# Kernel tuning notes

Measured on AMD Instinct MI355X. Metric: run time of the kernel, lower is better.

## Reference

```python
import jax, jax.numpy as jnp
import numpy as np

HS = WS = 1024      # downsampled mask dims (8192 / scale_factor 8)
K = 24              # kernel_num
KD = 35             # kernel_dim1 == kernel_dim2
OFF = HS // 2 - KD // 2  # offset_s = 495
MASK_STEEP = 4.0
MASK_SHIFT = 0.5
RESIST_STEEP = 50.0
RESIST_TH = 0.225
MAX_DOSE = 1.02
MIN_DOSE = 0.98
POOL = 3            # avepool_kernel


def setup_inputs() -> dict:
    key = jax.random.key(0)
    ks = jax.random.split(key, 7)
    return {
        "mask_s": jax.random.uniform(ks[0], (1, 1, HS, WS), dtype=jnp.float32),
        "kf_re": jax.random.normal(ks[1], (K, KD, KD), dtype=jnp.float32),
        "kf_im": jax.random.normal(ks[2], (K, KD, KD), dtype=jnp.float32),
        "kd_re": jax.random.normal(ks[3], (K, KD, KD), dtype=jnp.float32),
        "kd_im": jax.random.normal(ks[4], (K, KD, KD), dtype=jnp.float32),
        "kf_scale": jax.random.uniform(ks[5], (K, 1, 1), dtype=jnp.float32),
        "kd_scale": jax.random.uniform(ks[6], (K, 1, 1), dtype=jnp.float32),
    }


def _avgpool3(x):
    # AvgPool2d(kernel=3, stride=1, pad=1), count_include_pad=True -> always /9
    s = jax.lax.reduce_window(x, 0.0, jax.lax.add, (1, 1, POOL, POOL),
                              (1, 1, 1, 1),
                              [(0, 0), (0, 0), (POOL // 2, POOL // 2), (POOL // 2, POOL // 2)])
    return s / float(POOL * POOL)


def _dose_branch(crop, kernel, scale, dose):
    # crop: [1,1,KD,KD] complex ; kernel: [K,KD,KD] complex ; scale: [K,1,1]
    buf = jnp.zeros((1, K, HS, WS), dtype=jnp.complex64)
    buf = buf.at[:, :, OFF:OFF + KD, OFF:OFF + KD].set(crop * dose * kernel)
    img = jnp.fft.ifft2(buf)                      # [1,K,HS,WS] complex
    inten = (img.real * img.real + img.imag * img.imag) * scale
    inten = jnp.sum(inten, axis=1, keepdims=True)  # [1,1,HS,WS]
    return jax.nn.sigmoid(RESIST_STEEP * (inten - RESIST_TH))


def reference(mask_s, kf_re, kf_im, kd_re, kd_im, kf_scale, kd_scale):
    kf = jax.lax.complex(kf_re, kf_im)
    kd = jax.lax.complex(kd_re, kd_im)
    mask = jax.nn.sigmoid(MASK_STEEP * (_avgpool3(mask_s) - MASK_SHIFT))
    mf = jnp.fft.fftshift(jnp.fft.fft2(mask), axes=(-2, -1))  # [1,1,HS,WS]
    crop = mf[:, :, OFF:OFF + KD, OFF:OFF + KD]               # [1,1,KD,KD]
    x_nom = _dose_branch(crop, kf, kf_scale, 1.0)
    x_max = _dose_branch(crop, kf, kf_scale, MAX_DOSE)
    x_min = _dose_branch(crop, kd, kd_scale, MIN_DOSE)
    return x_nom, x_max, x_min
```

## Files before the change

kernel.cpp:

```cpp
#include <hip/hip_runtime.h>
#include <math.h>

#define HS 1024
#define WS 1024
#define KK 24
#define KD 35
#define NF 35
#define NDP 69
#define NGRP 16
#define CROW 42
#define PROW 37

#define G_OFF    0u
#define CROP_OFF 286720u
#define D_OFF    296520u
#define ZERO_QWORDS 6055

__global__ __launch_bounds__(256) void k_maskG(const float* __restrict__ ms,
                                               float2* __restrict__ G,
                                               unsigned long long* __restrict__ zq) {
    __shared__ float cs[WS + 8];
    __shared__ float m[WS];
    __shared__ float2 part[252];
    const int x = blockIdx.x;
    const int t = threadIdx.x;

    if (x < 24) {
        int i = x * 256 + t;
        if (i < ZERO_QWORDS) zq[i] = 0ull;
    }
    {
        const int j = 4 * t;
        float4 b = *(const float4*)&ms[x * WS + j];
        float4 a = make_float4(0.f, 0.f, 0.f, 0.f);
        float4 d = make_float4(0.f, 0.f, 0.f, 0.f);
        if (x > 0)      a = *(const float4*)&ms[(x - 1) * WS + j];
        if (x < HS - 1) d = *(const float4*)&ms[(x + 1) * WS + j];
        float4 s;
        s.x = a.x + b.x + d.x;
        s.y = a.y + b.y + d.y;
        s.z = a.z + b.z + d.z;
        s.w = a.w + b.w + d.w;
        *(float4*)&cs[4 + j] = s;
        if (t == 0) { cs[3] = 0.0f; cs[4 + WS] = 0.0f; }
    }
    __syncthreads();
    {
        const int j = 4 * t;
        float4 c = *(const float4*)&cs[4 + j];
        float l = cs[3 + j];
        float r = cs[8 + j];
        float p0 = (l   + c.x + c.y) * (1.0f / 9.0f);
        float p1 = (c.x + c.y + c.z) * (1.0f / 9.0f);
        float p2 = (c.y + c.z + c.w) * (1.0f / 9.0f);
        float p3 = (c.z + c.w + r  ) * (1.0f / 9.0f);
        float4 mv;
        mv.x = 1.0f / (1.0f + expf(-4.0f * (p0 - 0.5f)));
        mv.y = 1.0f / (1.0f + expf(-4.0f * (p1 - 0.5f)));
        mv.z = 1.0f / (1.0f + expf(-4.0f * (p2 - 0.5f)));
        mv.w = 1.0f / (1.0f + expf(-4.0f * (p3 - 0.5f)));
        *(float4*)&m[j] = mv;
    }
    __syncthreads();
    if (t < 252) {
        const int qi = t / 14, seg = t % 14;
        float si, ci, ss, cc;
        sincospif(-(float)(qi * seg) * (1.0f / 512.0f), &si, &ci);
        sincospif(-(float)(qi * 14)  * (1.0f / 512.0f), &ss, &cc);
        const float s2 = (qi & 1) ? -1.0f : 1.0f;
        const int qm = qi & 3;
        const float er = (qm == 0) ? 1.0f : (qm == 2) ? -1.0f : 0.0f;
        const float ei = (qm == 1) ? -1.0f : (qm == 3) ? 1.0f : 0.0f;
        float wr = ci, wi = si;
        float re = 0.0f, im = 0.0f;
        for (int y = seg; y < 256; y += 14) {
            float m0 = m[y], m1 = m[y + 256], m2 = m[y + 512], m3 = m[y + 768];
            float A  = fmaf(s2, m2, m0);
            float Bv = fmaf(s2, m3, m1);
            float tre = fmaf(er, Bv, A);
            float tim = ei * Bv;
            re += tre * wr - tim * wi;
            im += tre * wi + tim * wr;
            float nr = wr * cc - wi * ss;
            wi = wr * ss + wi * cc;
            wr = nr;
        }
        part[t] = make_float2(re, im);
    }
    __syncthreads();
    if (t < 18) {
        float re = 0.0f, im = 0.0f;
        for (int s = 0; s < 14; ++s) { float2 p = part[t * 14 + s]; re += p.x; im += p.y; }
        G[(17 + t) * HS + x] = make_float2(re, im);
        if (t > 0) G[(17 - t) * HS + x] = make_float2(re, -im);
    }
}

__global__ __launch_bounds__(256) void k_crop(const float2* __restrict__ G,
                                              float2* __restrict__ crop) {
    __shared__ float2 g2[64];
    __shared__ float2 part[245];
    const int q  = blockIdx.x >> 4;
    const int xs = (blockIdx.x & 15) * 64;
    const int t  = threadIdx.x;
    if (t < 64) g2[t] = G[q * HS + xs + t];
    __syncthreads();
    if (t < 245) {
        const int p = t / 7, seg = t % 7;
        const int v = p - 17;
        float si, ci, ss, cc;
        sincospif((float)(v * (xs + seg)) * (1.0f / 512.0f), &si, &ci);
        sincospif((float)(v * 7)          * (1.0f / 512.0f), &ss, &cc);
        float wr = ci, wi = si;
        float re = 0.0f, im = 0.0f;
        for (int r = seg; r < 64; r += 7) {
            float2 gv = g2[r];
            re += gv.x * wr + gv.y * wi;
            im += gv.y * wr - gv.x * wi;
            float nr = wr * cc - wi * ss;
            wi = wr * ss + wi * cc;
            wr = nr;
        }
        part[t] = make_float2(re, im);
    }
    __syncthreads();
    if (t < NF) {
        float re = 0.0f, im = 0.0f;
        for (int s = 0; s < 7; ++s) { float2 p2 = part[t * 7 + s]; re += p2.x; im += p2.y; }
        float* dst = (float*)&crop[t * NF + q];
        atomicAdd(dst,     re);
        atomicAdd(dst + 1, im);
    }
}

__global__ __launch_bounds__(256) void k_D(
    const float2* __restrict__ crop,
    const float* __restrict__ kre0, const float* __restrict__ kim0,
    const float* __restrict__ kre1, const float* __restrict__ kim1,
    const float* __restrict__ sc0,  const float* __restrict__ sc1,
    float2* __restrict__ D)
{
    __shared__ float2 C[KD * CROW];
    __shared__ float2 partR[2][28 * PROW];
    const int tup = blockIdx.x;
    const int t   = threadIdx.x;

    const int b   = tup / (KK * NGRP);
    const int rem = tup % (KK * NGRP);
    const int k   = rem / NGRP;
    const int g   = rem % NGRP;
    const float* kre = b ? kre1 : kre0;
    const float* kim = b ? kim1 : kim0;
    const float dosefac = (b ? 0.98f : 1.0f) * (1.0f / 1048576.0f);
    const float sk2 = ((b ? sc1 : sc0)[k]) * dosefac * dosefac;

    if (t < 245) C[(t / 7) * CROW + 35 + (t % 7)] = make_float2(0.0f, 0.0f);
    #pragma unroll
    for (int j = 0; j < 5; ++j) {
        int i = t + j * 256;
        if (i < KD * KD) {
            float2 c = crop[i];
            int row = i / 35, col = i % 35;
            float kr = kre[k * KD * KD + i], ki = kim[k * KD * KD + i];
            C[row * CROW + col] = make_float2(c.x * kr - c.y * ki,
                                              c.x * ki + c.y * kr);
        }
    }
    __syncthreads();

    const int tile = t / 28;
    const int r    = t % 28;
    const int pgrp = r / 7;
    const int useg = r % 7;
    const int d0   = tile * 4;
    const int u0   = useg * 5;

    int pb = 0;
    for (int idp = g; idp < NDP; idp += NGRP) {
        const int dp = idp - 34;
        if (t < 252) {
            const int plo = max(0, dp), phi = min(34, 34 + dp);
            float2 ac0 = {0,0}, ac1 = {0,0}, ac2 = {0,0}, ac3 = {0,0};
            if (u0 <= 34 - d0) {
                for (int p = plo + pgrp; p <= phi; p += 4) {
                    const float2* rowa = &C[p * CROW + d0 + u0];
                    const float2* rowb = &C[(p - dp) * CROW + u0];
                    float2 a0 = rowa[0], a1 = rowa[1], a2 = rowa[2];
                    #pragma unroll
                    for (int s = 0; s < 5; ++s) {
                        float2 a3 = rowa[s + 3];
                        float2 bb = rowb[s];
                        ac0.x += a0.x * bb.x + a0.y * bb.y;  ac0.y += a0.y * bb.x - a0.x * bb.y;
                        ac1.x += a1.x * bb.x + a1.y * bb.y;  ac1.y += a1.y * bb.x - a1.x * bb.y;
                        ac2.x += a2.x * bb.x + a2.y * bb.y;  ac2.y += a2.y * bb.x - a2.x * bb.y;
                        ac3.x += a3.x * bb.x + a3.y * bb.y;  ac3.y += a3.y * bb.x - a3.x * bb.y;
                        a0 = a1; a1 = a2; a2 = a3;
                    }
                }
            }
            const int base = r * PROW + d0;
            partR[pb][base]     = ac0;
            partR[pb][base + 1] = ac1;
            partR[pb][base + 2] = ac2;
            partR[pb][base + 3] = ac3;
        }
        __syncthreads();
        if (t < NF) {
            float re = 0.0f, im = 0.0f;
            for (int rr = 0; rr < 28; ++rr) {
                float2 v = partR[pb][rr * PROW + t];
                re += v.x; im += v.y;
            }
            float* dst = (float*)&D[(b * NDP + idp) * NF + t];
            atomicAdd(dst,     re * sk2);
            atomicAdd(dst + 1, im * sk2);
        }
        pb ^= 1;
    }
}

__global__ __launch_bounds__(256) void k_final(const float2* __restrict__ D,
                                               float* __restrict__ out) {
    __shared__ float2 partB[210];
    __shared__ float2 B[NF][2];
    const int x = blockIdx.x;
    const int t = threadIdx.x;
    if (t < 210) {
        const int s = t / 70, r = t % 70, b = r / 35, dq = r % 35;
        float si, ci, ss, cc;
        sincospif((float)((23 * s - 34) * x) * (1.0f / 512.0f), &si, &ci);
        sincospif((float)x                   * (1.0f / 512.0f), &ss, &cc);
        float wr = ci, wi = si;
        float re = 0.0f, im = 0.0f;
        const int i0 = 23 * s;
        for (int idp = i0; idp < i0 + 23; ++idp) {
            float2 d = D[(b * NDP + idp) * NF + dq];
            re += d.x * wr - d.y * wi;
            im += d.x * wi + d.y * wr;
            float nr = wr * cc - wi * ss;
            wi = wr * ss + wi * cc;
            wr = nr;
        }
        partB[t] = make_float2(re, im);
    }
    __syncthreads();
    if (t < 70) {
        float2 a = partB[t], b2 = partB[t + 70], c = partB[t + 140];
        B[t % 35][t / 35] = make_float2(a.x + b2.x + c.x, a.y + b2.y + c.y);
    }
    __syncthreads();
    const float bf0 = B[0][0].x;
    const float bd0 = B[0][1].x;
    float s1, c1;
    sincospif((float)t * (1.0f / 512.0f), &s1, &c1);
    float cx = c1, cy = s1;
    float2 Sf[4] = {{0,0},{0,0},{0,0},{0,0}};
    float2 Sd[4] = {{0,0},{0,0},{0,0},{0,0}};
    #pragma unroll
    for (int dq = 1; dq < NF; ++dq) {
        const float2 bf = B[dq][0];
        const float2 bd = B[dq][1];
        const int mm = dq & 3;
        Sf[mm].x += bf.x * cx - bf.y * cy;
        Sf[mm].y += bf.x * cy + bf.y * cx;
        Sd[mm].x += bd.x * cx - bd.y * cy;
        Sd[mm].y += bd.x * cy + bd.y * cx;
        const float nx = cx * c1 - cy * s1;
        cy = cx * s1 + cy * c1;
        cx = nx;
    }
    float sf[4], sd[4];
    sf[0] = Sf[0].x + Sf[1].x + Sf[2].x + Sf[3].x;
    sf[1] = Sf[0].x - Sf[1].y - Sf[2].x + Sf[3].y;
    sf[2] = Sf[0].x - Sf[1].x + Sf[2].x - Sf[3].x;
    sf[3] = Sf[0].x + Sf[1].y - Sf[2].x - Sf[3].y;
    sd[0] = Sd[0].x + Sd[1].x + Sd[2].x + Sd[3].x;
    sd[1] = Sd[0].x - Sd[1].y - Sd[2].x + Sd[3].y;
    sd[2] = Sd[0].x - Sd[1].x + Sd[2].x - Sd[3].x;
    sd[3] = Sd[0].x + Sd[1].y - Sd[2].x - Sd[3].y;
    #pragma unroll
    for (int j = 0; j < 4; ++j) {
        const float If = bf0 + 2.0f * sf[j];
        const float Id = bd0 + 2.0f * sd[j];
        const int o = x * WS + t + 256 * j;
        out[o]               = 1.0f / (1.0f + expf(-50.0f * (If - 0.225f)));
        out[o + HS * WS]     = 1.0f / (1.0f + expf(-50.0f * (1.0404f * If - 0.225f)));
        out[o + 2 * HS * WS] = 1.0f / (1.0f + expf(-50.0f * (Id - 0.225f)));
    }
}

extern "C" void kernel_launch(void* const* d_in, const int* in_sizes, int n_in,
                              void* d_out, int out_size, void* d_ws, size_t ws_size,
                              hipStream_t stream) {
    (void)in_sizes; (void)n_in; (void)out_size; (void)ws_size;
    const float* ms    = (const float*)d_in[0];
    const float* kf_re = (const float*)d_in[1];
    const float* kf_im = (const float*)d_in[2];
    const float* kd_re = (const float*)d_in[3];
    const float* kd_im = (const float*)d_in[4];
    const float* kf_sc = (const float*)d_in[5];
    const float* kd_sc = (const float*)d_in[6];

    char* ws = (char*)d_ws;
    float2* G      = (float2*)(ws + G_OFF);
    float2* crop   = (float2*)(ws + CROP_OFF);
    float2* D      = (float2*)(ws + D_OFF);
    unsigned long long* zq = (unsigned long long*)(ws + CROP_OFF);
    float* out     = (float*)d_out;

    k_maskG<<<HS, 256, 0, stream>>>(ms, G, zq);
    k_crop<<<NF * 16, 256, 0, stream>>>(G, crop);
    k_D<<<2 * KK * NGRP, 256, 0, stream>>>(crop, kf_re, kf_im, kd_re, kd_im, kf_sc, kd_sc, D);
    k_final<<<HS, 256, 0, stream>>>(D, out);
}
```

Before: 51.65 us.

## Remap k_D thread work to only valid triangular chunks with six p-groups

Reassigns threads in the correlation kernel so that only the 38 valid (diagonal tile, u-segment) chunks in the triangular region are active, each split across six p-groups instead of four. This removes idle threads that previously skipped work because u0 exceeded 34-d0, and shortens each thread's p loop. The reduction step now sums a variable number of partials per output column from a flat per-thread buffer, which adds index arithmetic and possible LDS bank conflicts.

```diff
diff --git a/kernel.cpp b/kernel.cpp
--- a/kernel.cpp
+++ b/kernel.cpp
@@ -9,7 +9,8 @@
 #define NDP 69
 #define NGRP 16
 #define CROW 42
-#define PROW 37
+#define NCHUNK 38
+#define PRS 10
 
 #define G_OFF    0u
 #define CROP_OFF 286720u
@@ -141,7 +142,7 @@
     float2* __restrict__ D)
 {
     __shared__ float2 C[KD * CROW];
-    __shared__ float2 partR[2][28 * PROW];
+    __shared__ float partRf[2][NCHUNK * 6 * PRS];
     const int tup = blockIdx.x;
     const int t   = threadIdx.x;
 
@@ -168,47 +169,55 @@
     }
     __syncthreads();
 
-    const int tile = t / 28;
-    const int r    = t % 28;
-    const int pgrp = r / 7;
-    const int useg = r % 7;
-    const int d0   = tile * 4;
-    const int u0   = useg * 5;
+    const int ch = t / 6;
+    const int pg = t % 6;
+    const bool act = (ch < NCHUNK);
+    const int tau = (ch >= 7) + (ch >= 14) + (ch >= 20) + (ch >= 25)
+                  + (ch >= 29) + (ch >= 32) + (ch >= 35) + (ch >= 37);
+    const int cbt = (tau == 0) ? 0 : (tau == 1) ? 7 : (tau == 2) ? 14 : (tau == 3) ? 20
+                  : (tau == 4) ? 25 : (tau == 5) ? 29 : (tau == 6) ? 32 : (tau == 7) ? 35 : 37;
+    const int d0 = 4 * tau;
+    const int u0 = 5 * (ch - cbt);
+
+    const int tau2 = t >> 2;
+    const int cb2 = (tau2 == 0) ? 0 : (tau2 == 1) ? 7 : (tau2 == 2) ? 14 : (tau2 == 3) ? 20
+                  : (tau2 == 4) ? 25 : (tau2 == 5) ? 29 : (tau2 == 6) ? 32 : (tau2 == 7) ? 35 : 37;
+    const int cn2 = (tau2 == 0) ? 7 : (tau2 == 1) ? 7 : (tau2 == 2) ? 6 : (tau2 == 3) ? 5
+                  : (tau2 == 4) ? 4 : (tau2 == 5) ? 3 : (tau2 == 6) ? 3 : (tau2 == 7) ? 2 : 1;
+    const int s0 = cb2 * 6, cnt = cn2 * 6, c2 = (t & 3) * 2;
 
     int pb = 0;
     for (int idp = g; idp < NDP; idp += NGRP) {
         const int dp = idp - 34;
-        if (t < 252) {
+        if (act) {
             const int plo = max(0, dp), phi = min(34, 34 + dp);
             float2 ac0 = {0,0}, ac1 = {0,0}, ac2 = {0,0}, ac3 = {0,0};
-            if (u0 <= 34 - d0) {
-                for (int p = plo + pgrp; p <= phi; p += 4) {
-                    const float2* rowa = &C[p * CROW + d0 + u0];
-                    const float2* rowb = &C[(p - dp) * CROW + u0];
-                    float2 a0 = rowa[0], a1 = rowa[1], a2 = rowa[2];
-                    #pragma unroll
-                    for (int s = 0; s < 5; ++s) {
-                        float2 a3 = rowa[s + 3];
-                        float2 bb = rowb[s];
-                        ac0.x += a0.x * bb.x + a0.y * bb.y;  ac0.y += a0.y * bb.x - a0.x * bb.y;
-                        ac1.x += a1.x * bb.x + a1.y * bb.y;  ac1.y += a1.y * bb.x - a1.x * bb.y;
-                        ac2.x += a2.x * bb.x + a2.y * bb.y;  ac2.y += a2.y * bb.x - a2.x * bb.y;
-                        ac3.x += a3.x * bb.x + a3.y * bb.y;  ac3.y += a3.y * bb.x - a3.x * bb.y;
-                        a0 = a1; a1 = a2; a2 = a3;
-                    }
+            for (int p = plo + pg; p <= phi; p += 6) {
+                const float2* rowa = &C[p * CROW + d0 + u0];
+                const float2* rowb = &C[(p - dp) * CROW + u0];
+                float2 a0 = rowa[0], a1 = rowa[1], a2 = rowa[2];
+                #pragma unroll
+                for (int s = 0; s < 5; ++s) {
+                    float2 a3 = rowa[s + 3];
+                    float2 bb = rowb[s];
+                    ac0.x += a0.x * bb.x + a0.y * bb.y;  ac0.y += a0.y * bb.x - a0.x * bb.y;
+                    ac1.x += a1.x * bb.x + a1.y * bb.y;  ac1.y += a1.y * bb.x - a1.x * bb.y;
+                    ac2.x += a2.x * bb.x + a2.y * bb.y;  ac2.y += a2.y * bb.x - a2.x * bb.y;
+                    ac3.x += a3.x * bb.x + a3.y * bb.y;  ac3.y += a3.y * bb.x - a3.x * bb.y;
+                    a0 = a1; a1 = a2; a2 = a3;
                 }
             }
-            const int base = r * PROW + d0;
-            partR[pb][base]     = ac0;
-            partR[pb][base + 1] = ac1;
-            partR[pb][base + 2] = ac2;
-            partR[pb][base + 3] = ac3;
+            float* pr = &partRf[pb][t * PRS];
+            *(float2*)&pr[0] = ac0;
+            *(float2*)&pr[2] = ac1;
+            *(float2*)&pr[4] = ac2;
+            *(float2*)&pr[6] = ac3;
         }
         __syncthreads();
         if (t < NF) {
             float re = 0.0f, im = 0.0f;
-            for (int rr = 0; rr < 28; ++rr) {
-                float2 v = partR[pb][rr * PROW + t];
+            for (int j = 0; j < cnt; ++j) {
+                const float2 v = *(const float2*)&partRf[pb][(s0 + j) * PRS + c2];
                 re += v.x; im += v.y;
             }
             float* dst = (float*)&D[(b * NDP + idp) * NF + t];
```

Result: faster. 48.94 us (median of 2 runs) (-5.3%).
